# Kernel optimization log

Hardware: AMD Instinct MI355X
Metric: run time of the kernel (lower is better)

The kernel has to match this reference:

```python
import jax, jax.numpy as jnp
import numpy as np


NUM_HEADS = 16


def setup_inputs() -> dict:
    key = jax.random.key(0)
    ks = jax.random.split(key, 6)
    B, Sq, Skv, DQ, DKV = 2, 1024, 4096, 1024, 768
    return {
        "x_q": jax.random.normal(ks[0], (B, Sq, DQ), jnp.float32),
        "x_kv": jax.random.normal(ks[1], (B, Skv, DKV), jnp.float32),
        "Wq": jax.random.normal(ks[2], (DQ, DQ), jnp.float32) * 0.02,
        "Wk": jax.random.normal(ks[3], (DQ, DKV), jnp.float32) * 0.02,
        "Wv": jax.random.normal(ks[4], (DQ, DKV), jnp.float32) * 0.02,
        "Wo": jax.random.normal(ks[5], (DQ, DQ), jnp.float32) * 0.02,
    }


def _split_heads(x):
    # Faithful to torch view(B, H, S, hd): a pure reshape, NOT a transpose.
    B, S, D = x.shape
    return x.reshape(B, NUM_HEADS, S, D // NUM_HEADS)


def reference(x_q, x_kv, Wq, Wk, Wv, Wo):
    head_dim = x_q.shape[-1] // NUM_HEADS
    # torch Linear: y = x @ W.T, weight shape (out, in)
    Q = _split_heads(jnp.einsum("bsd,od->bso", x_q, Wq))   # (B,H,Sq',hd)
    K = _split_heads(jnp.einsum("bsd,od->bso", x_kv, Wk))  # (B,H,Skv',hd)
    V = _split_heads(jnp.einsum("bsd,od->bso", x_kv, Wv))
    # Scale is 1/head_dim (not 1/sqrt), faithful to the source.
    scores = jnp.einsum("bhqd,bhkd->bhqk", Q, K) / head_dim
    attn = jax.nn.softmax(scores, axis=-1)
    out = jnp.einsum("bhqk,bhkd->bhqd", attn, V)  # (B,H,Sq',hd)
    B, Sq, DQ = x_q.shape
    out = out.transpose(0, 2, 1, 3).reshape(B, Sq, DQ)
    return jnp.einsum("bsd,od->bso", out, Wo)
```

## Files before the change

### kernel.cpp

```cpp
#include <hip/hip_runtime.h>
#include <hip/hip_bf16.h>
#include <cstdint>

#define THREADS 256

typedef __attribute__((ext_vector_type(8))) short bf16x8;
typedef __attribute__((ext_vector_type(4))) float f32x4;

__device__ __forceinline__ void load_lds16(const void* g, void* l) {
    __builtin_amdgcn_global_load_lds(
        (const __attribute__((address_space(1))) unsigned int*)g,
        (__attribute__((address_space(3))) unsigned int*)l, 16, 0, 0);
}

__device__ __forceinline__ unsigned short f2bf(float x) {
    __hip_bfloat16 hb = __float2bfloat16(x);
    return *(unsigned short*)&hb;
}

__global__ __launch_bounds__(THREADS)
void cast_inputs(const float* __restrict__ xq, const float* __restrict__ xkv,
                 const float* __restrict__ wq, const float* __restrict__ wk,
                 const float* __restrict__ wv, const float* __restrict__ wo,
                 unsigned short* __restrict__ oq, unsigned short* __restrict__ okv,
                 unsigned short* __restrict__ owq, unsigned short* __restrict__ owk,
                 unsigned short* __restrict__ owv, unsigned short* __restrict__ owo) {
    const unsigned n0 = 524288, n1 = 1572864, n2 = 262144, n3 = 196608, n4 = 196608;
    unsigned i = blockIdx.x * THREADS + threadIdx.x;
    const float* src; unsigned short* dst; unsigned off;
    if (i < n0)                    { src = xq;  dst = oq;  off = i; }
    else if (i < n0+n1)            { src = xkv; dst = okv; off = i - n0; }
    else if (i < n0+n1+n2)         { src = wq;  dst = owq; off = i - n0 - n1; }
    else if (i < n0+n1+n2+n3)      { src = wk;  dst = owk; off = i - n0 - n1 - n2; }
    else if (i < n0+n1+n2+n3+n4)   { src = wv;  dst = owv; off = i - n0 - n1 - n2 - n3; }
    else                           { src = wo;  dst = owo; off = i - n0 - n1 - n2 - n3 - n4; }
    float4 v = *(const float4*)(src + (size_t)off * 4);
    ushort4 o;
    o.x = f2bf(v.x); o.y = f2bf(v.y); o.z = f2bf(v.z); o.w = f2bf(v.w);
    *(ushort4*)(dst + (size_t)off * 4) = o;
}

__global__ __launch_bounds__(THREADS)
void gemm_proj(const unsigned short* __restrict__ xkv, const unsigned short* __restrict__ wkv,
               unsigned short* __restrict__ Kn, unsigned short* __restrict__ Vt,
               const unsigned short* __restrict__ xq, const unsigned short* __restrict__ wq,
               unsigned short* __restrict__ Qout) {
    __shared__ __align__(16) unsigned short As[128 * 64];
    __shared__ __align__(16) unsigned short Bs[128 * 64];

    const int t    = threadIdx.x;
    const int w    = t >> 6;
    const int lane = t & 63;
    const int l15  = lane & 15;
    const int quad = lane >> 4;
    const int wm   = w & 1;
    const int wn   = w >> 1;

    if (blockIdx.x < 1024) {
        const int bN = (blockIdx.x & 15) * 128;
        const int bM = (blockIdx.x >> 4) * 128;
        const int Kd = 768;

        const int srow = t >> 3;
        const int scol = ((t & 7) ^ ((t >> 4) & 7)) << 3;
        const unsigned short* ga = xkv + (size_t)(bM + srow) * Kd + scol;
        const unsigned short* gb = wkv + (size_t)(bN + srow) * Kd + scol;
        const int lbase = w * 512;

        const int xr = (l15 >> 1) & 7;
        int aoff[2][4], boff[2][4];
#pragma unroll
        for (int kk = 0; kk < 2; ++kk)
#pragma unroll
            for (int mt = 0; mt < 4; ++mt) {
                aoff[kk][mt] = (wm * 64 + mt * 16 + l15) * 64 + (((kk * 4 + quad) ^ xr) << 3);
                boff[kk][mt] = (wn * 64 + mt * 16 + l15) * 64 + (((kk * 4 + quad) ^ xr) << 3);
            }

        f32x4 acc[4][4];
#pragma unroll
        for (int mt = 0; mt < 4; ++mt)
#pragma unroll
            for (int nt = 0; nt < 4; ++nt)
#pragma unroll
                for (int r = 0; r < 4; ++r) acc[mt][nt][r] = 0.f;

        for (int k0 = 0; k0 < Kd; k0 += 64) {
            __syncthreads();
#pragma unroll
            for (int it = 0; it < 4; ++it) {
                load_lds16(ga + (size_t)it * 32 * Kd + k0, &As[lbase + it * 2048]);
                load_lds16(gb + (size_t)it * 32 * Kd + k0, &Bs[lbase + it * 2048]);
            }
            __syncthreads();

#pragma unroll
            for (int kk = 0; kk < 2; ++kk) {
                bf16x8 af[4], bf[4];
#pragma unroll
                for (int mt = 0; mt < 4; ++mt) af[mt] = *(const bf16x8*)&As[aoff[kk][mt]];
#pragma unroll
                for (int nt = 0; nt < 4; ++nt) bf[nt] = *(const bf16x8*)&Bs[boff[kk][nt]];
#pragma unroll
                for (int mt = 0; mt < 4; ++mt)
#pragma unroll
                    for (int nt = 0; nt < 4; ++nt)
                        acc[mt][nt] = __builtin_amdgcn_mfma_f32_16x16x32_bf16(af[mt], bf[nt], acc[mt][nt], 0, 0, 0);
            }
        }

        const int rbase = bM + wm * 64;
        const int b  = rbase >> 12;
        const int h  = (rbase & 4095) >> 8;
        if (bN < 1024) {
            const int G = (bN + wn * 64) >> 6;
            unsigned short* kp = Kn + (size_t)(b * 16 + h) * 262144 + (size_t)G * 256 * 64 + l15;
#pragma unroll
            for (int mt = 0; mt < 4; ++mt)
#pragma unroll
                for (int r = 0; r < 4; ++r) {
                    int u = (rbase & 255) + mt * 16 + quad * 4 + r;
                    unsigned short* cp = kp + (size_t)u * 64;
#pragma unroll
                    for (int nt = 0; nt < 4; ++nt) cp[nt * 16] = f2bf(acc[mt][nt][r]);
                }
        } else {
            const int Gv = (bN - 1024 + wn * 64) >> 6;
            unsigned short* vp = Vt + (size_t)(b * 16 + h) * 262144 + (size_t)Gv * 256;
#pragma unroll
            for (int nt = 0; nt < 4; ++nt) {
                int d = nt * 16 + l15;
#pragma unroll
                for (int mt = 0; mt < 4; ++mt) {
                    int u = (rbase & 255) + mt * 16 + quad * 4;
                    ushort4 pk;
                    pk.x = f2bf(acc[mt][nt][0]);
                    pk.y = f2bf(acc[mt][nt][1]);
                    pk.z = f2bf(acc[mt][nt][2]);
                    pk.w = f2bf(acc[mt][nt][3]);
                    *(ushort4*)(vp + (size_t)d * 4096 + u) = pk;
                }
            }
        }
    } else {
        const int id = blockIdx.x - 1024;
        const int bN = (id & 15) * 64;
        const int bM = (id >> 4) * 64;
        const int Kd = 1024, N = 1024;

        const int srow = t >> 3;
        const int scol = ((t & 7) ^ ((t >> 3) & 7)) << 3;
        const unsigned short* ga = xq + (size_t)(bM + srow) * Kd + scol;
        const unsigned short* gb = wq + (size_t)(bN + srow) * Kd + scol;
        const int lbase = w * 512;

        int aoff[2][2], boff[2][2];
#pragma unroll
        for (int kk = 0; kk < 2; ++kk)
#pragma unroll
            for (int mt = 0; mt < 2; ++mt) {
                aoff[kk][mt] = (wm * 32 + mt * 16 + l15) * 64 + (((kk * 4 + quad) ^ (l15 & 7)) << 3);
                boff[kk][mt] = (wn * 32 + mt * 16 + l15) * 64 + (((kk * 4 + quad) ^ (l15 & 7)) << 3);
            }

        f32x4 acc[2][2];
#pragma unroll
        for (int mt = 0; mt < 2; ++mt)
#pragma unroll
            for (int nt = 0; nt < 2; ++nt)
#pragma unroll
                for (int r = 0; r < 4; ++r) acc[mt][nt][r] = 0.f;

        for (int k0 = 0; k0 < Kd; k0 += 64) {
            __syncthreads();
#pragma unroll
            for (int it = 0; it < 2; ++it) {
                load_lds16(ga + (size_t)it * 32 * Kd + k0, &As[lbase + it * 2048]);
                load_lds16(gb + (size_t)it * 32 * Kd + k0, &Bs[lbase + it * 2048]);
            }
            __syncthreads();

#pragma unroll
            for (int kk = 0; kk < 2; ++kk) {
                bf16x8 af[2], bf[2];
#pragma unroll
                for (int mt = 0; mt < 2; ++mt) af[mt] = *(const bf16x8*)&As[aoff[kk][mt]];
#pragma unroll
                for (int nt = 0; nt < 2; ++nt) bf[nt] = *(const bf16x8*)&Bs[boff[kk][nt]];
#pragma unroll
                for (int mt = 0; mt < 2; ++mt)
#pragma unroll
                    for (int nt = 0; nt < 2; ++nt)
                        acc[mt][nt] = __builtin_amdgcn_mfma_f32_16x16x32_bf16(af[mt], bf[nt], acc[mt][nt], 0, 0, 0);
            }
        }

#pragma unroll
        for (int mt = 0; mt < 2; ++mt)
#pragma unroll
            for (int r = 0; r < 4; ++r) {
                int row = bM + wm * 32 + mt * 16 + quad * 4 + r;
                int col = bN + wn * 32 + l15;
                unsigned short* cp = Qout + (size_t)row * N + col;
#pragma unroll
                for (int nt = 0; nt < 2; ++nt) cp[nt * 16] = f2bf(acc[mt][nt][r]);
            }
    }
}

template <bool OUTF32>
__global__ __launch_bounds__(THREADS)
void gemm_bf16_nt64(const unsigned short* __restrict__ A, const unsigned short* __restrict__ W,
                    void* __restrict__ Cout, int M, int N, int Kd) {
    __shared__ __align__(16) unsigned short As[64 * 64];
    __shared__ __align__(16) unsigned short Bs[64 * 64];

    const int t    = threadIdx.x;
    const int w    = t >> 6;
    const int lane = t & 63;
    const int l15  = lane & 15;
    const int quad = lane >> 4;
    const int wm   = w & 1;
    const int wn   = w >> 1;
    const int bM = blockIdx.y * 64;
    const int bN = blockIdx.x * 64;

    const int srow = t >> 3;
    const int scol = ((t & 7) ^ ((t >> 3) & 7)) << 3;
    const unsigned short* ga = A + (size_t)(bM + srow) * Kd + scol;
    const unsigned short* gb = W + (size_t)(bN + srow) * Kd + scol;
    const int lbase = w * 512;

    int aoff[2][2], boff[2][2];
#pragma unroll
    for (int kk = 0; kk < 2; ++kk)
#pragma unroll
        for (int mt = 0; mt < 2; ++mt) {
            aoff[kk][mt] = (wm * 32 + mt * 16 + l15) * 64 + (((kk * 4 + quad) ^ (l15 & 7)) << 3);
            boff[kk][mt] = (wn * 32 + mt * 16 + l15) * 64 + (((kk * 4 + quad) ^ (l15 & 7)) << 3);
        }

    f32x4 acc[2][2];
#pragma unroll
    for (int mt = 0; mt < 2; ++mt)
#pragma unroll
        for (int nt = 0; nt < 2; ++nt)
#pragma unroll
            for (int r = 0; r < 4; ++r) acc[mt][nt][r] = 0.f;

    for (int k0 = 0; k0 < Kd; k0 += 64) {
        __syncthreads();
#pragma unroll
        for (int it = 0; it < 2; ++it) {
            load_lds16(ga + (size_t)it * 32 * Kd + k0, &As[lbase + it * 2048]);
            load_lds16(gb + (size_t)it * 32 * Kd + k0, &Bs[lbase + it * 2048]);
        }
        __syncthreads();

#pragma unroll
        for (int kk = 0; kk < 2; ++kk) {
            bf16x8 af[2], bf[2];
#pragma unroll
            for (int mt = 0; mt < 2; ++mt) af[mt] = *(const bf16x8*)&As[aoff[kk][mt]];
#pragma unroll
            for (int nt = 0; nt < 2; ++nt) bf[nt] = *(const bf16x8*)&Bs[boff[kk][nt]];
#pragma unroll
            for (int mt = 0; mt < 2; ++mt)
#pragma unroll
                for (int nt = 0; nt < 2; ++nt)
                    acc[mt][nt] = __builtin_amdgcn_mfma_f32_16x16x32_bf16(af[mt], bf[nt], acc[mt][nt], 0, 0, 0);
        }
    }

#pragma unroll
    for (int mt = 0; mt < 2; ++mt)
#pragma unroll
        for (int r = 0; r < 4; ++r) {
            int row = bM + wm * 32 + mt * 16 + quad * 4 + r;
            int col = bN + wn * 32 + l15;
            if (OUTF32) {
                float* cp = (float*)Cout + (size_t)row * N + col;
#pragma unroll
                for (int nt = 0; nt < 2; ++nt) cp[nt * 16] = acc[mt][nt][r];
            } else {
                unsigned short* cp = (unsigned short*)Cout + (size_t)row * N + col;
#pragma unroll
                for (int nt = 0; nt < 2; ++nt) cp[nt * 16] = f2bf(acc[mt][nt][r]);
            }
        }
}

__global__ __launch_bounds__(THREADS, 2)
void attn_mfma8(const unsigned short* __restrict__ Q, const unsigned short* __restrict__ K,
                const unsigned short* __restrict__ Vt, unsigned short* __restrict__ AO) {
    extern __shared__ __align__(16) unsigned short sm[];
    unsigned short* Ks = sm;
    unsigned short* Vs = sm + 8192;
    unsigned short* Ps = sm + 16384;
    float* OS = (float*)sm;
    float* Lw = (float*)(sm + 26624);

    const int bid  = blockIdx.x;
    const int slot = bid >> 3;
    const int qq   = slot & 15;
    const int hh   = (bid & 7) + 8 * (slot >> 4);
    const int q0 = qq * 64;
    const int h  = hh & 15;
    const int b  = hh >> 4;

    const int t    = threadIdx.x;
    const int w    = t >> 6;
    const int lane = t & 63;
    const int l15  = lane & 15;
    const int quad = lane >> 4;

    const unsigned short* Qh = Q + (size_t)b * 1048576 + (size_t)h * 65536 + (size_t)q0 * 64;
    const unsigned short* Kh = K + (size_t)b * 4194304 + (size_t)h * 262144;
    const unsigned short* Vh = Vt + (size_t)(b * 16 + h) * 262144;

    bf16x8 Qb[4][2];
#pragma unroll
    for (int qt = 0; qt < 4; ++qt)
#pragma unroll
        for (int kk = 0; kk < 2; ++kk)
            Qb[qt][kk] = *(const bf16x8*)(Qh + (size_t)(qt * 16 + l15) * 64 + kk * 32 + quad * 8);

    const unsigned short* gKw = Kh + (size_t)(w * 32 + (lane >> 3)) * 64
                                   + (((lane & 7) ^ ((lane >> 3) & 7)) << 3);
    const unsigned short* gVw = Vh + (size_t)(lane >> 2) * 4096 + w * 32
                                   + (((lane & 3) ^ ((lane >> 2) & 3)) << 3);
    const int ldsK = w * 2048;
    const int ldsV = w * 2048;

    int koff[2][2];
#pragma unroll
    for (int kvt = 0; kvt < 2; ++kvt)
#pragma unroll
        for (int kk = 0; kk < 2; ++kk)
            koff[kvt][kk] = (w * 32 + kvt * 16 + l15) * 64 + (((kk * 4 + quad) ^ (l15 & 7)) << 3);
    int voff[4];
#pragma unroll
    for (int dt = 0; dt < 4; ++dt)
        voff[dt] = w * 2048 + (dt * 16 + l15) * 32 + ((quad ^ (l15 & 3)) << 3);

    const int pw  = w * 2560;
    const int pq  = pw + l15 * 40;

    f32x4 Oacc[4][4];
#pragma unroll
    for (int qt = 0; qt < 4; ++qt)
#pragma unroll
        for (int dt = 0; dt < 4; ++dt)
#pragma unroll
            for (int r = 0; r < 4; ++r) Oacc[qt][dt][r] = 0.f;
    float lsum[4] = {0.f, 0.f, 0.f, 0.f};

    const float scale = 1.0f / 64.0f;

    for (int kc = 0; kc < 32; ++kc) {
#pragma unroll
        for (int it = 0; it < 4; ++it)
            load_lds16(gKw + (size_t)kc * 8192 + it * 512, &Ks[ldsK + it * 512]);
#pragma unroll
        for (int it = 0; it < 4; ++it)
            load_lds16(gVw + (size_t)kc * 128 + (size_t)it * 65536, &Vs[ldsV + it * 512]);
        asm volatile("s_waitcnt vmcnt(0)" ::: "memory");

#pragma unroll
        for (int kvt = 0; kvt < 2; ++kvt) {
            bf16x8 ka = *(const bf16x8*)&Ks[koff[kvt][0]];
            bf16x8 kb = *(const bf16x8*)&Ks[koff[kvt][1]];
#pragma unroll
            for (int qt = 0; qt < 4; ++qt) {
                f32x4 S = {0.f, 0.f, 0.f, 0.f};
                S = __builtin_amdgcn_mfma_f32_16x16x32_bf16(ka, Qb[qt][0], S, 0, 0, 0);
                S = __builtin_amdgcn_mfma_f32_16x16x32_bf16(kb, Qb[qt][1], S, 0, 0, 0);
                float p0 = __expf(S[0] * scale);
                float p1 = __expf(S[1] * scale);
                float p2 = __expf(S[2] * scale);
                float p3 = __expf(S[3] * scale);
                lsum[qt] += (p0 + p1) + (p2 + p3);
                ushort4 pk4;
                pk4.x = f2bf(p0); pk4.y = f2bf(p1); pk4.z = f2bf(p2); pk4.w = f2bf(p3);
                *(ushort4*)&Ps[pq + qt * 640 + kvt * 16 + quad * 4] = pk4;
            }
        }

        bf16x8 Vf[4];
#pragma unroll
        for (int dt = 0; dt < 4; ++dt) Vf[dt] = *(const bf16x8*)&Vs[voff[dt]];
        asm volatile("s_waitcnt lgkmcnt(0)" ::: "memory");

#pragma unroll
        for (int qt = 0; qt < 4; ++qt) {
            bf16x8 Pa = *(const bf16x8*)&Ps[pq + qt * 640 + quad * 8];
#pragma unroll
            for (int dt = 0; dt < 4; ++dt)
                Oacc[qt][dt] = __builtin_amdgcn_mfma_f32_16x16x32_bf16(Pa, Vf[dt], Oacc[qt][dt], 0, 0, 0);
        }
    }

#pragma unroll
    for (int qt = 0; qt < 4; ++qt) {
        float v = lsum[qt];
        v += __shfl_xor(v, 16);
        v += __shfl_xor(v, 32);
        lsum[qt] = v;
    }
    __syncthreads();
    if (lane < 16) {
#pragma unroll
        for (int qt = 0; qt < 4; ++qt)
            Lw[w * 64 + qt * 16 + lane] = lsum[qt];
    }
    if (w > 0) {
        float* myOS = OS + (w - 1) * 4352;
#pragma unroll
        for (int qt = 0; qt < 4; ++qt)
#pragma unroll
            for (int dt = 0; dt < 4; ++dt)
                *(f32x4*)&myOS[(dt * 16 + l15) * 68 + qt * 16 + quad * 4] = Oacc[qt][dt];
    }
    __syncthreads();
    if (w == 0) {
#pragma unroll
        for (int qt = 0; qt < 4; ++qt) {
            f32x4 lv = *(const f32x4*)&Lw[qt * 16 + quad * 4];
            lv += *(const f32x4*)&Lw[64 + qt * 16 + quad * 4];
            lv += *(const f32x4*)&Lw[128 + qt * 16 + quad * 4];
            lv += *(const f32x4*)&Lw[192 + qt * 16 + quad * 4];
            f32x4 inv;
#pragma unroll
            for (int r = 0; r < 4; ++r) inv[r] = 1.0f / lv[r];
#pragma unroll
            for (int dt = 0; dt < 4; ++dt) {
                f32x4 o = Oacc[qt][dt];
                int os = (dt * 16 + l15) * 68 + qt * 16 + quad * 4;
                o += *(const f32x4*)&OS[os];
                o += *(const f32x4*)&OS[4352 + os];
                o += *(const f32x4*)&OS[8704 + os];
#pragma unroll
                for (int r = 0; r < 4; ++r) {
                    int q = qt * 16 + quad * 4 + r;
                    AO[(size_t)b * 1048576 + (size_t)(q0 + q) * 1024 + (h << 6) + dt * 16 + l15]
                        = f2bf(o[r] * inv[r]);
                }
            }
        }
    }
}

extern "C" void kernel_launch(void* const* d_in, const int* in_sizes, int n_in,
                              void* d_out, int out_size, void* d_ws, size_t ws_size,
                              hipStream_t stream) {
    const float* x_q  = (const float*)d_in[0];
    const float* x_kv = (const float*)d_in[1];
    const float* Wq   = (const float*)d_in[2];
    const float* Wk   = (const float*)d_in[3];
    const float* Wv   = (const float*)d_in[4];
    const float* Wo   = (const float*)d_in[5];
    float* out = (float*)d_out;

    unsigned short* base   = (unsigned short*)d_ws;
    unsigned short* xq_bf  = base;
    unsigned short* xkv_bf = base + 2097152;
    unsigned short* wq_bf  = base + 8388608;
    unsigned short* wk_bf  = base + 9437184;
    unsigned short* wv_bf  = base + 10223616;
    unsigned short* wo_bf  = base + 11010048;
    unsigned short* Qw     = base + 12058624;
    unsigned short* Kw     = base + 14155776;
    unsigned short* AOb    = base + 22544384;
    unsigned short* Vtw    = base + 30932992;

    dim3 blk(THREADS);
    cast_inputs<<<dim3(11776), blk, 0, stream>>>(x_q, x_kv, Wq, Wk, Wv, Wo,
                                                 xq_bf, xkv_bf, wq_bf, wk_bf, wv_bf, wo_bf);
    gemm_proj<<<dim3(1536), blk, 0, stream>>>(xkv_bf, wk_bf, Kw, Vtw, xq_bf, wq_bf, Qw);
    attn_mfma8<<<dim3(512), blk, 54272, stream>>>(Qw, Kw, Vtw, AOb);
    gemm_bf16_nt64<true><<<dim3(16, 32), blk, 0, stream>>>(AOb, wo_bf, (void*)out, 2048, 1024, 1024);
}
```

Before: 205.2 us.

## Prefetch next K/V chunk into LDS while computing current attention chunk

Restructures the attention KV loop into a software pipeline. The K and V loads for the next chunk are issued straight after the current chunk's fragments have been read from LDS, and partial vmcnt waits replace the full drain. The goal is to hide global-load latency behind the QK^T and PV MFMA work. It reuses single LDS buffers per wave, so correctness depends on the wait ordering. It also issues one redundant wraparound load on the last iteration.

```diff
diff --git a/kernel.cpp b/kernel.cpp
--- a/kernel.cpp
+++ b/kernel.cpp
@@ -291,7 +291,7 @@
 }
 
 __global__ __launch_bounds__(THREADS, 2)
-void attn_mfma8(const unsigned short* __restrict__ Q, const unsigned short* __restrict__ K,
+void attn_mfma9(const unsigned short* __restrict__ Q, const unsigned short* __restrict__ K,
                 const unsigned short* __restrict__ Vt, unsigned short* __restrict__ AO) {
     extern __shared__ __align__(16) unsigned short sm[];
     unsigned short* Ks = sm;
@@ -357,47 +357,69 @@
 
     const float scale = 1.0f / 64.0f;
 
+#pragma unroll
+    for (int it = 0; it < 4; ++it)
+        load_lds16(gKw + it * 512, &Ks[ldsK + it * 512]);
+#pragma unroll
+    for (int it = 0; it < 4; ++it)
+        load_lds16(gVw + (size_t)it * 65536, &Vs[ldsV + it * 512]);
+
     for (int kc = 0; kc < 32; ++kc) {
+        const int kn = (kc + 1) & 31;
+
+        asm volatile("s_waitcnt vmcnt(4)" ::: "memory");
+
+        bf16x8 ka0 = *(const bf16x8*)&Ks[koff[0][0]];
+        bf16x8 kb0 = *(const bf16x8*)&Ks[koff[0][1]];
+        bf16x8 ka1 = *(const bf16x8*)&Ks[koff[1][0]];
+        bf16x8 kb1 = *(const bf16x8*)&Ks[koff[1][1]];
+        asm volatile("s_waitcnt lgkmcnt(0)" ::: "memory");
 #pragma unroll
         for (int it = 0; it < 4; ++it)
-            load_lds16(gKw + (size_t)kc * 8192 + it * 512, &Ks[ldsK + it * 512]);
+            load_lds16(gKw + (size_t)kn * 8192 + it * 512, &Ks[ldsK + it * 512]);
+
+#pragma unroll
+        for (int qt = 0; qt < 4; ++qt) {
+            f32x4 S0 = {0.f, 0.f, 0.f, 0.f};
+            S0 = __builtin_amdgcn_mfma_f32_16x16x32_bf16(ka0, Qb[qt][0], S0, 0, 0, 0);
+            S0 = __builtin_amdgcn_mfma_f32_16x16x32_bf16(kb0, Qb[qt][1], S0, 0, 0, 0);
+            f32x4 S1 = {0.f, 0.f, 0.f, 0.f};
+            S1 = __builtin_amdgcn_mfma_f32_16x16x32_bf16(ka1, Qb[qt][0], S1, 0, 0, 0);
+            S1 = __builtin_amdgcn_mfma_f32_16x16x32_bf16(kb1, Qb[qt][1], S1, 0, 0, 0);
+            float p0 = __expf(S0[0] * scale);
+            float p1 = __expf(S0[1] * scale);
+            float p2 = __expf(S0[2] * scale);
+            float p3 = __expf(S0[3] * scale);
+            float p4 = __expf(S1[0] * scale);
+            float p5 = __expf(S1[1] * scale);
+            float p6 = __expf(S1[2] * scale);
+            float p7 = __expf(S1[3] * scale);
+            lsum[qt] += ((p0 + p1) + (p2 + p3)) + ((p4 + p5) + (p6 + p7));
+            ushort4 pk4a, pk4b;
+            pk4a.x = f2bf(p0); pk4a.y = f2bf(p1); pk4a.z = f2bf(p2); pk4a.w = f2bf(p3);
+            pk4b.x = f2bf(p4); pk4b.y = f2bf(p5); pk4b.z = f2bf(p6); pk4b.w = f2bf(p7);
+            *(ushort4*)&Ps[pq + qt * 640 + quad * 4]      = pk4a;
+            *(ushort4*)&Ps[pq + qt * 640 + 16 + quad * 4] = pk4b;
+        }
+
+        asm volatile("s_waitcnt vmcnt(4)" ::: "memory");
+        asm volatile("s_waitcnt lgkmcnt(0)" ::: "memory");
+
+        bf16x8 Vf[4], Pa[4];
+#pragma unroll
+        for (int dt = 0; dt < 4; ++dt) Vf[dt] = *(const bf16x8*)&Vs[voff[dt]];
+#pragma unroll
+        for (int qt = 0; qt < 4; ++qt) Pa[qt] = *(const bf16x8*)&Ps[pq + qt * 640 + quad * 8];
+        asm volatile("s_waitcnt lgkmcnt(0)" ::: "memory");
 #pragma unroll
         for (int it = 0; it < 4; ++it)
-            load_lds16(gVw + (size_t)kc * 128 + (size_t)it * 65536, &Vs[ldsV + it * 512]);
-        asm volatile("s_waitcnt vmcnt(0)" ::: "memory");
-
-#pragma unroll
-        for (int kvt = 0; kvt < 2; ++kvt) {
-            bf16x8 ka = *(const bf16x8*)&Ks[koff[kvt][0]];
-            bf16x8 kb = *(const bf16x8*)&Ks[koff[kvt][1]];
-#pragma unroll
-            for (int qt = 0; qt < 4; ++qt) {
-                f32x4 S = {0.f, 0.f, 0.f, 0.f};
-                S = __builtin_amdgcn_mfma_f32_16x16x32_bf16(ka, Qb[qt][0], S, 0, 0, 0);
-                S = __builtin_amdgcn_mfma_f32_16x16x32_bf16(kb, Qb[qt][1], S, 0, 0, 0);
-                float p0 = __expf(S[0] * scale);
-                float p1 = __expf(S[1] * scale);
-                float p2 = __expf(S[2] * scale);
-                float p3 = __expf(S[3] * scale);
-                lsum[qt] += (p0 + p1) + (p2 + p3);
-                ushort4 pk4;
-                pk4.x = f2bf(p0); pk4.y = f2bf(p1); pk4.z = f2bf(p2); pk4.w = f2bf(p3);
-                *(ushort4*)&Ps[pq + qt * 640 + kvt * 16 + quad * 4] = pk4;
-            }
-        }
-
-        bf16x8 Vf[4];
-#pragma unroll
-        for (int dt = 0; dt < 4; ++dt) Vf[dt] = *(const bf16x8*)&Vs[voff[dt]];
-        asm volatile("s_waitcnt lgkmcnt(0)" ::: "memory");
-
-#pragma unroll
-        for (int qt = 0; qt < 4; ++qt) {
-            bf16x8 Pa = *(const bf16x8*)&Ps[pq + qt * 640 + quad * 8];
+            load_lds16(gVw + (size_t)kn * 128 + (size_t)it * 65536, &Vs[ldsV + it * 512]);
+
+#pragma unroll
+        for (int qt = 0; qt < 4; ++qt)
 #pragma unroll
             for (int dt = 0; dt < 4; ++dt)
-                Oacc[qt][dt] = __builtin_amdgcn_mfma_f32_16x16x32_bf16(Pa, Vf[dt], Oacc[qt][dt], 0, 0, 0);
-        }
+                Oacc[qt][dt] = __builtin_amdgcn_mfma_f32_16x16x32_bf16(Pa[qt], Vf[dt], Oacc[qt][dt], 0, 0, 0);
     }
 
 #pragma unroll
@@ -477,6 +499,6 @@
     cast_inputs<<<dim3(11776), blk, 0, stream>>>(x_q, x_kv, Wq, Wk, Wv, Wo,
                                                  xq_bf, xkv_bf, wq_bf, wk_bf, wv_bf, wo_bf);
     gemm_proj<<<dim3(1536), blk, 0, stream>>>(xkv_bf, wk_bf, Kw, Vtw, xq_bf, wq_bf, Qw);
-    attn_mfma8<<<dim3(512), blk, 54272, stream>>>(Qw, Kw, Vtw, AOb);
+    attn_mfma9<<<dim3(512), blk, 54272, stream>>>(Qw, Kw, Vtw, AOb);
     gemm_bf16_nt64<true><<<dim3(16, 32), blk, 0, stream>>>(AOb, wo_bf, (void*)out, 2048, 1024, 1024);
 }
```

Result: no change. 201.2 us (-1.9%).
